# Performance work log

Measured on AMD Instinct MI355X. Metric: run time of the kernel, lower is better.

Reference implementation:

```python
import jax, jax.numpy as jnp
import numpy as np

CHANNELS, STYLE_DIM, N_HEADS, N_TOK = 512, 256, 2, 50
HEAD_DIM = STYLE_DIM // N_HEADS
SCALE = STYLE_DIM ** (-0.5)


def setup_inputs() -> dict:
    key = jax.random.key(0)
    ks = jax.random.split(key, 12)
    B, T = 16, 4096
    s = lambda fan_in: 1.0 / np.sqrt(fan_in)
    return {
        "x": jax.random.normal(ks[0], (B, CHANNELS, T), jnp.float32),
        "style": jax.random.normal(ks[1], (B, N_TOK, STYLE_DIM), jnp.float32),
        "key_emb": jax.random.normal(ks[2], (1, N_TOK, STYLE_DIM), jnp.float32) * 0.3,
        "Wq": jax.random.uniform(ks[3], (STYLE_DIM, CHANNELS), jnp.float32, -s(CHANNELS), s(CHANNELS)),
        "bq": jax.random.uniform(ks[4], (STYLE_DIM,), jnp.float32, -s(CHANNELS), s(CHANNELS)),
        "Wk": jax.random.uniform(ks[5], (STYLE_DIM, STYLE_DIM), jnp.float32, -s(STYLE_DIM), s(STYLE_DIM)),
        "bk": jax.random.uniform(ks[6], (STYLE_DIM,), jnp.float32, -s(STYLE_DIM), s(STYLE_DIM)),
        "Wv": jax.random.uniform(ks[7], (STYLE_DIM, STYLE_DIM), jnp.float32, -s(STYLE_DIM), s(STYLE_DIM)),
        "bv": jax.random.uniform(ks[8], (STYLE_DIM,), jnp.float32, -s(STYLE_DIM), s(STYLE_DIM)),
        "Wo": jax.random.uniform(ks[9], (CHANNELS, STYLE_DIM), jnp.float32, -s(STYLE_DIM), s(STYLE_DIM)),
        "bo": jax.random.uniform(ks[10], (CHANNELS,), jnp.float32, -s(STYLE_DIM), s(STYLE_DIM)),
    }


def reference(x, style, key_emb, Wq, bq, Wk, bk, Wv, bv, Wo, bo):
    B, C, T = x.shape
    N = style.shape[1]
    # Q from x (transposed to [B,T,C]); K from static learned embedding; V from style
    q = jnp.einsum('bct,dc->btd', x, Wq) + bq                 # [B,T,style_dim]
    k = jnp.einsum('bns,ds->bnd', jnp.broadcast_to(key_emb, (B, N_TOK, STYLE_DIM)), Wk) + bk
    v = jnp.einsum('bns,ds->bnd', style, Wv) + bv
    # split heads: [B,H,T,hd] / [B,H,N,hd]
    q = q.reshape(B, T, N_HEADS, HEAD_DIM).transpose(0, 2, 1, 3)
    k = k.reshape(B, N_TOK, N_HEADS, HEAD_DIM).transpose(0, 2, 1, 3)
    v = v.reshape(B, N, N_HEADS, HEAD_DIM).transpose(0, 2, 1, 3)
    # tanh applied to transposed keys before QK^T
    attn = jnp.einsum('bhtd,bhnd->bhtn', q, jnp.tanh(k)) * SCALE
    attn = jax.nn.softmax(attn, axis=-1)
    out = jnp.einsum('bhtn,bhnd->bhtd', attn, v)              # [B,H,T,hd]
    out = out.transpose(0, 2, 1, 3).reshape(B, T, STYLE_DIM)
    out = jnp.einsum('btd,cd->btc', out, Wo) + bo             # [B,T,C]
    return x + out.transpose(0, 2, 1)
```

## Files before the change

### kernel.cpp

```cpp
#include <hip/hip_runtime.h>
#include <stdint.h>

#define CHN 512
#define TDIM 4096
#define SD 256
#define HD 128
#define NTOK 50
#define NP 64
#define NB 16
#define TT 64
#define QPITCH 264
#define XPITCH 132
#define SCALE_ 0.0625f

typedef float f32x4 __attribute__((ext_vector_type(4)));
typedef unsigned int u32x4 __attribute__((ext_vector_type(4)));
typedef short s16x8 __attribute__((ext_vector_type(8)));

__device__ __forceinline__ uint16_t f2bf(float f) {
  union { float f; uint32_t u; } v; v.f = f;
  uint32_t r = (v.u + 0x7fffu + ((v.u >> 16) & 1u)) >> 16;
  return (uint16_t)r;
}
__device__ __forceinline__ uint32_t packbf(float lo, float hi) {
  return (uint32_t)f2bf(lo) | ((uint32_t)f2bf(hi) << 16);
}
__device__ __forceinline__ void mfma_bf16(f32x4& d, u32x4 a, u32x4 b) {
  union { u32x4 u; s16x8 s; } ua, ub;
  ua.u = a; ub.u = b;
  d = __builtin_amdgcn_mfma_f32_16x16x32_bf16(ua.s, ub.s, d, 0, 0, 0);
}

__global__ void conv_w_kernel(const float* __restrict__ Wq, const float* __restrict__ Wo,
                              uint16_t* __restrict__ wqb, uint16_t* __restrict__ wob) {
  int i = blockIdx.x * 256 + threadIdx.x;
  wqb[i] = f2bf(Wq[i]);
  wob[i] = f2bf(Wo[i]);
}

__global__ void prep_kv_kernel(const float* __restrict__ style, const float* __restrict__ kemb,
                               const float* __restrict__ Wk, const float* __restrict__ bk,
                               const float* __restrict__ Wv, const float* __restrict__ bv,
                               uint16_t* __restrict__ kt, uint16_t* __restrict__ vT) {
  int id = blockIdx.x * 256 + threadIdx.x;
  if (id < 2 * NP * HD) {
    int dh = id & (HD - 1);
    int n  = (id >> 7) & (NP - 1);
    int h  = id >> 13;
    uint16_t r = 0;
    if (n < NTOK) {
      int d = h * HD + dh;
      float acc = bk[d];
      const float* er = kemb + (size_t)n * SD;
      const float* wr = Wk + (size_t)d * SD;
      for (int s = 0; s < SD; s += 4) {
        float4 e = *(const float4*)(er + s);
        float4 w4 = *(const float4*)(wr + s);
        acc += e.x * w4.x + e.y * w4.y + e.z * w4.z + e.w * w4.w;
      }
      r = f2bf(tanhf(acc));
    }
    kt[id] = r;
  } else {
    int vid = id - 2 * NP * HD;
    int n  = vid & (NP - 1);
    int dh = (vid >> 6) & (HD - 1);
    int h  = (vid >> 13) & 1;
    int bb = vid >> 14;
    uint16_t r = 0;
    if (n < NTOK) {
      int d = h * HD + dh;
      float acc = bv[d];
      const float* sr = style + (size_t)(bb * NTOK + n) * SD;
      const float* wr = Wv + (size_t)d * SD;
      for (int s = 0; s < SD; s += 4) {
        float4 e = *(const float4*)(sr + s);
        float4 w4 = *(const float4*)(wr + s);
        acc += e.x * w4.x + e.y * w4.y + e.z * w4.z + e.w * w4.w;
      }
      r = f2bf(acc);
    }
    vT[vid] = r;
  }
}

__global__ __launch_bounds__(256, 2) void fused_kernel(
    const float* __restrict__ x, const float* __restrict__ bq, const float* __restrict__ bo,
    const uint16_t* __restrict__ wqb, const uint16_t* __restrict__ wob,
    const uint16_t* __restrict__ kt, const uint16_t* __restrict__ vT,
    float* __restrict__ out) {
  __shared__ uint16_t qs[TT * QPITCH];

  const int bb = blockIdx.y;
  const int t0 = blockIdx.x * TT;
  const int tid = threadIdx.x;
  const int lane = tid & 63;
  const int w = tid >> 6;
  const int l15 = lane & 15;
  const int g = lane >> 4;

  const float* xb = x + (size_t)bb * CHN * TDIM + t0;

  f32x4 acc[4][4];
#pragma unroll
  for (int mt = 0; mt < 4; ++mt)
#pragma unroll
    for (int nt = 0; nt < 4; ++nt) acc[mt][nt] = (f32x4){0.f, 0.f, 0.f, 0.f};

  const int tse = (tid & 31) << 1;
  const int cb  = (tid >> 5) << 1;

  float2 va[8], vb[8];
#pragma unroll
  for (int p = 0; p < 8; ++p) {
    int c = cb + 16 * p;
    va[p] = *(const float2*)(xb + (size_t)c * TDIM + tse);
    vb[p] = *(const float2*)(xb + (size_t)(c + 1) * TDIM + tse);
  }

  for (int cc = 0; cc < 4; ++cc) {
    const int c0 = cc * 128;
    __syncthreads();
#pragma unroll
    for (int p = 0; p < 8; ++p) {
      int cl = cb + 16 * p;
      *(uint32_t*)&qs[tse * XPITCH + cl]       = packbf(va[p].x, vb[p].x);
      *(uint32_t*)&qs[(tse + 1) * XPITCH + cl] = packbf(va[p].y, vb[p].y);
    }
    if (cc < 3) {
      const int c0n = c0 + 128;
#pragma unroll
      for (int p = 0; p < 8; ++p) {
        int c = c0n + cb + 16 * p;
        va[p] = *(const float2*)(xb + (size_t)c * TDIM + tse);
        vb[p] = *(const float2*)(xb + (size_t)(c + 1) * TDIM + tse);
      }
    }
    __syncthreads();
#pragma unroll
    for (int ks = 0; ks < 4; ++ks) {
      u32x4 afr[4];
#pragma unroll
      for (int mt = 0; mt < 4; ++mt) {
        int dr = (w * 4 + mt) * 16 + l15;
        afr[mt] = *(const u32x4*)(wqb + (size_t)dr * CHN + c0 + ks * 32 + g * 8);
      }
#pragma unroll
      for (int nt = 0; nt < 4; ++nt) {
        int tr = nt * 16 + l15;
        const uint16_t* pb = &qs[tr * XPITCH + ks * 32 + g * 8];
        uint2 lo = *(const uint2*)pb;
        uint2 hi = *(const uint2*)(pb + 4);
        u32x4 bfr = (u32x4){lo.x, lo.y, hi.x, hi.y};
#pragma unroll
        for (int mt = 0; mt < 4; ++mt) mfma_bf16(acc[mt][nt], afr[mt], bfr);
      }
    }
  }
  __syncthreads();
#pragma unroll
  for (int mt = 0; mt < 4; ++mt) {
    int d0 = (w * 4 + mt) * 16 + g * 4;
    float4 bqv = *(const float4*)(bq + d0);
#pragma unroll
    for (int nt = 0; nt < 4; ++nt) {
      int tr = nt * 16 + l15;
      uint2 wv;
      wv.x = packbf(acc[mt][nt][0] + bqv.x, acc[mt][nt][1] + bqv.y);
      wv.y = packbf(acc[mt][nt][2] + bqv.z, acc[mt][nt][3] + bqv.w);
      *(uint2*)&qs[tr * QPITCH + d0] = wv;
    }
  }
  __syncthreads();

  const int tmy = w * 16 + l15;
  const uint16_t* qrow = &qs[tmy * QPITCH];
  const int l1 = l15 + 16 * ((2 * g) & 3);
  const int l2 = l15 + 16 * ((2 * g + 1) & 3);
  const bool hiH = (g >> 1) != 0;

#pragma unroll
  for (int h = 0; h < 2; ++h) {
    u32x4 bq4[4];
#pragma unroll
    for (int ks = 0; ks < 4; ++ks)
      bq4[ks] = *(const u32x4*)(qrow + h * HD + ks * 32 + g * 8);

    f32x4 sac[4];
#pragma unroll
    for (int mtn = 0; mtn < 4; ++mtn) {
      sac[mtn] = (f32x4){0.f, 0.f, 0.f, 0.f};
#pragma unroll
      for (int ks = 0; ks < 4; ++ks) {
        u32x4 afr = *(const u32x4*)(kt + (size_t)(h * NP + mtn * 16 + l15) * HD + ks * 32 + g * 8);
        mfma_bf16(sac[mtn], afr, bq4[ks]);
      }
    }
    float pv[4][4];
    float mx = -3.0e38f;
#pragma unroll
    for (int mtn = 0; mtn < 4; ++mtn)
#pragma unroll
      for (int j = 0; j < 4; ++j) {
        int n = mtn * 16 + g * 4 + j;
        float s = (n < NTOK) ? sac[mtn][j] * SCALE_ : -3.0e38f;
        pv[mtn][j] = s;
        mx = fmaxf(mx, s);
      }
    mx = fmaxf(mx, __shfl_xor(mx, 16, 64));
    mx = fmaxf(mx, __shfl_xor(mx, 32, 64));
    float sum = 0.f;
#pragma unroll
    for (int mtn = 0; mtn < 4; ++mtn)
#pragma unroll
      for (int j = 0; j < 4; ++j) {
        float e = __expf(pv[mtn][j] - mx);
        pv[mtn][j] = e;
        sum += e;
      }
    sum += __shfl_xor(sum, 16, 64);
    sum += __shfl_xor(sum, 32, 64);
    float inv = 1.0f / sum;
    uint32_t pk[4][2];
#pragma unroll
    for (int mtn = 0; mtn < 4; ++mtn) {
      pk[mtn][0] = packbf(pv[mtn][0] * inv, pv[mtn][1] * inv);
      pk[mtn][1] = packbf(pv[mtn][2] * inv, pv[mtn][3] * inv);
    }
    u32x4 bp[2];
#pragma unroll
    for (int ks = 0; ks < 2; ++ks) {
      uint32_t a0 = (uint32_t)__shfl((int)pk[2 * ks][0], l1, 64);
      uint32_t b0 = (uint32_t)__shfl((int)pk[2 * ks + 1][0], l1, 64);
      uint32_t a1 = (uint32_t)__shfl((int)pk[2 * ks][1], l1, 64);
      uint32_t b1 = (uint32_t)__shfl((int)pk[2 * ks + 1][1], l1, 64);
      uint32_t a2 = (uint32_t)__shfl((int)pk[2 * ks][0], l2, 64);
      uint32_t b2 = (uint32_t)__shfl((int)pk[2 * ks + 1][0], l2, 64);
      uint32_t a3 = (uint32_t)__shfl((int)pk[2 * ks][1], l2, 64);
      uint32_t b3 = (uint32_t)__shfl((int)pk[2 * ks + 1][1], l2, 64);
      bp[ks] = (u32x4){hiH ? b0 : a0, hiH ? b1 : a1, hiH ? b2 : a2, hiH ? b3 : a3};
    }
    const uint16_t* vb2 = vT + (size_t)((bb * 2 + h) * HD) * NP;
#pragma unroll
    for (int mtd = 0; mtd < 8; ++mtd) {
      f32x4 oac = (f32x4){0.f, 0.f, 0.f, 0.f};
#pragma unroll
      for (int ks = 0; ks < 2; ++ks) {
        u32x4 afr = *(const u32x4*)(vb2 + (size_t)(mtd * 16 + l15) * NP + ks * 32 + g * 8);
        mfma_bf16(oac, afr, bp[ks]);
      }
      int d0 = h * HD + mtd * 16 + g * 4;
      uint2 wv;
      wv.x = packbf(oac[0], oac[1]);
      wv.y = packbf(oac[2], oac[3]);
      *(uint2*)&qs[tmy * QPITCH + d0] = wv;
    }
  }

  u32x4 ak[8];
#pragma unroll
  for (int ks = 0; ks < 8; ++ks)
    ak[ks] = *(const u32x4*)(qrow + ks * 32 + g * 8);

  const float* xr = x + (size_t)bb * CHN * TDIM;
  float* orow = out + (size_t)bb * CHN * TDIM;
  const int t4 = t0 + w * 16 + g * 4;

  float4 xg[8];
#pragma unroll
  for (int i = 0; i < 8; ++i) {
    int c = i * 16 + l15;
    xg[i] = *(const float4*)(xr + (size_t)c * TDIM + t4);
  }
#pragma unroll
  for (int nt = 0; nt < 32; ++nt) {
    int c = nt * 16 + l15;
    const uint16_t* wrow = wob + (size_t)c * SD;
    f32x4 yac = (f32x4){0.f, 0.f, 0.f, 0.f};
#pragma unroll
    for (int ks = 0; ks < 8; ++ks) {
      u32x4 bfr = *(const u32x4*)(wrow + ks * 32 + g * 8);
      mfma_bf16(yac, ak[ks], bfr);
    }
    float bov = bo[c];
    float4 xv = xg[nt & 7];
    if (nt + 8 < 32) {
      int c2 = (nt + 8) * 16 + l15;
      xg[nt & 7] = *(const float4*)(xr + (size_t)c2 * TDIM + t4);
    }
    float4 ov;
    ov.x = xv.x + yac[0] + bov;
    ov.y = xv.y + yac[1] + bov;
    ov.z = xv.z + yac[2] + bov;
    ov.w = xv.w + yac[3] + bov;
    *(float4*)(orow + (size_t)c * TDIM + t4) = ov;
  }
}

extern "C" void kernel_launch(void* const* d_in, const int* in_sizes, int n_in,
                              void* d_out, int out_size, void* d_ws, size_t ws_size,
                              hipStream_t stream) {
  const float* x     = (const float*)d_in[0];
  const float* style = (const float*)d_in[1];
  const float* kemb  = (const float*)d_in[2];
  const float* Wq    = (const float*)d_in[3];
  const float* bq    = (const float*)d_in[4];
  const float* Wk    = (const float*)d_in[5];
  const float* bk    = (const float*)d_in[6];
  const float* Wv    = (const float*)d_in[7];
  const float* bv    = (const float*)d_in[8];
  const float* Wo    = (const float*)d_in[9];
  const float* bo    = (const float*)d_in[10];
  float* out = (float*)d_out;

  uint16_t* wqb = (uint16_t*)d_ws;
  uint16_t* wob = wqb + 131072;
  uint16_t* ktw = wob + 131072;
  uint16_t* vTw = ktw + 16384;

  conv_w_kernel<<<512, 256, 0, stream>>>(Wq, Wo, wqb, wob);
  prep_kv_kernel<<<1088, 256, 0, stream>>>(style, kemb, Wk, bk, Wv, bv, ktw, vTw);
  dim3 grid(TDIM / TT, NB);
  fused_kernel<<<grid, 256, 0, stream>>>(x, bq, bo, wqb, wob, ktw, vTw, out);
}
```

Baseline: 253.2 us.

## Split fused kernel into Q-projection/attention and output-projection kernels

Splits the single fused kernel into two launches. The first computes the Q projection and attention and writes the bf16 attention output to a global workspace buffer. The second reads that buffer, applies the output projection and adds the residual, loading x directly each iteration instead of through a software-prefetched register ring. The aim is likely to cut register pressure and raise occupancy in each stage, at the cost of an extra global round trip (16x4096x256 bf16), a second read of x, and an extra launch.

```diff
diff --git a/kernel.cpp b/kernel.cpp
--- a/kernel.cpp
+++ b/kernel.cpp
@@ -84,11 +84,11 @@
   }
 }
 
-__global__ __launch_bounds__(256, 2) void fused_kernel(
-    const float* __restrict__ x, const float* __restrict__ bq, const float* __restrict__ bo,
-    const uint16_t* __restrict__ wqb, const uint16_t* __restrict__ wob,
+__global__ __launch_bounds__(256, 2) void qproj_attn_kernel(
+    const float* __restrict__ x, const float* __restrict__ bq,
+    const uint16_t* __restrict__ wqb,
     const uint16_t* __restrict__ kt, const uint16_t* __restrict__ vT,
-    float* __restrict__ out) {
+    uint16_t* __restrict__ o) {
   __shared__ uint16_t qs[TT * QPITCH];
 
   const int bb = blockIdx.y;
@@ -175,6 +175,7 @@
 
   const int tmy = w * 16 + l15;
   const uint16_t* qrow = &qs[tmy * QPITCH];
+  uint16_t* og = o + (size_t)(bb * TDIM + t0 + tmy) * SD;
   const int l1 = l15 + 16 * ((2 * g) & 3);
   const int l2 = l15 + 16 * ((2 * g + 1) & 3);
   const bool hiH = (g >> 1) != 0;
@@ -253,26 +254,35 @@
       uint2 wv;
       wv.x = packbf(oac[0], oac[1]);
       wv.y = packbf(oac[2], oac[3]);
-      *(uint2*)&qs[tmy * QPITCH + d0] = wv;
-    }
-  }
-
+      *(uint2*)(og + d0) = wv;
+    }
+  }
+}
+
+__global__ __launch_bounds__(256, 2) void oproj_kernel(
+    const float* __restrict__ x, const float* __restrict__ bo,
+    const uint16_t* __restrict__ wob, const uint16_t* __restrict__ o,
+    float* __restrict__ out) {
+  const int bb = blockIdx.y;
+  const int t0 = blockIdx.x * TT;
+  const int tid = threadIdx.x;
+  const int lane = tid & 63;
+  const int w = tid >> 6;
+  const int l15 = lane & 15;
+  const int g = lane >> 4;
+  const int tmy = w * 16 + l15;
+
+  const uint16_t* orow_in = o + (size_t)(bb * TDIM + t0 + tmy) * SD;
   u32x4 ak[8];
 #pragma unroll
   for (int ks = 0; ks < 8; ++ks)
-    ak[ks] = *(const u32x4*)(qrow + ks * 32 + g * 8);
+    ak[ks] = *(const u32x4*)(orow_in + ks * 32 + g * 8);
 
   const float* xr = x + (size_t)bb * CHN * TDIM;
   float* orow = out + (size_t)bb * CHN * TDIM;
   const int t4 = t0 + w * 16 + g * 4;
 
-  float4 xg[8];
-#pragma unroll
-  for (int i = 0; i < 8; ++i) {
-    int c = i * 16 + l15;
-    xg[i] = *(const float4*)(xr + (size_t)c * TDIM + t4);
-  }
-#pragma unroll
+#pragma unroll 4
   for (int nt = 0; nt < 32; ++nt) {
     int c = nt * 16 + l15;
     const uint16_t* wrow = wob + (size_t)c * SD;
@@ -283,11 +293,7 @@
       mfma_bf16(yac, ak[ks], bfr);
     }
     float bov = bo[c];
-    float4 xv = xg[nt & 7];
-    if (nt + 8 < 32) {
-      int c2 = (nt + 8) * 16 + l15;
-      xg[nt & 7] = *(const float4*)(xr + (size_t)c2 * TDIM + t4);
-    }
+    float4 xv = *(const float4*)(xr + (size_t)c * TDIM + t4);
     float4 ov;
     ov.x = xv.x + yac[0] + bov;
     ov.y = xv.y + yac[1] + bov;
@@ -317,9 +323,11 @@
   uint16_t* wob = wqb + 131072;
   uint16_t* ktw = wob + 131072;
   uint16_t* vTw = ktw + 16384;
+  uint16_t* ob  = vTw + 262144;
 
   conv_w_kernel<<<512, 256, 0, stream>>>(Wq, Wo, wqb, wob);
   prep_kv_kernel<<<1088, 256, 0, stream>>>(style, kemb, Wk, bk, Wv, bv, ktw, vTw);
   dim3 grid(TDIM / TT, NB);
-  fused_kernel<<<grid, 256, 0, stream>>>(x, bq, bo, wqb, wob, ktw, vTw, out);
-}
+  qproj_attn_kernel<<<grid, 256, 0, stream>>>(x, bq, wqb, ktw, vTw, ob);
+  oproj_kernel<<<grid, 256, 0, stream>>>(x, bo, wob, ob, out);
+}
```

Result: slower. 270.4 us (+6.8%).
